# Kernel optimization log

Measured on AMD Instinct MI355X. Metric: run time of the kernel, lower is better.

The kernel has to match this reference:

```python
import jax, jax.numpy as jnp
import numpy as np

B, T, C = 4, 2048, 768
N_HEAD = 12
HS = C // N_HEAD

def setup_inputs() -> dict:
    key = jax.random.key(0)
    ks = jax.random.split(key, 5)
    s = 0.02
    return {
        "x": jax.random.normal(ks[0], (B, T, C), dtype=jnp.float32),
        "w_attn": jax.random.normal(ks[1], (C, 3 * C), dtype=jnp.float32) * s,
        "b_attn": jnp.zeros((3 * C,), dtype=jnp.float32),
        "w_proj": jax.random.normal(ks[2], (C, C), dtype=jnp.float32) * s,
        "b_proj": jnp.zeros((C,), dtype=jnp.float32),
    }

def reference(x, w_attn, b_attn, w_proj, b_proj):
    Bx, Tx, Cx = x.shape
    qkv = x @ w_attn + b_attn                      # [B,T,3C]
    q, k, v = jnp.split(qkv, 3, axis=-1)
    # [B,H,T,hs]
    q = q.reshape(Bx, Tx, N_HEAD, HS).transpose(0, 2, 1, 3)
    k = k.reshape(Bx, Tx, N_HEAD, HS).transpose(0, 2, 1, 3)
    v = v.reshape(Bx, Tx, N_HEAD, HS).transpose(0, 2, 1, 3)
    att = jnp.einsum('bhqd,bhkd->bhqk', q, k) * (1.0 / jnp.sqrt(jnp.float32(HS)))
    mask = jnp.tril(jnp.ones((Tx, Tx), dtype=bool))  # causal
    att = jnp.where(mask, att, jnp.float32(-jnp.inf))
    att = jax.nn.softmax(att, axis=-1)
    y = jnp.einsum('bhqk,bhkd->bhqd', att, v)
    y = y.transpose(0, 2, 1, 3).reshape(Bx, Tx, Cx)
    return y @ w_proj + b_proj
```

## Files before the change

### kernel.cpp

```cpp
#include <hip/hip_runtime.h>

#define BB 4
#define TT 2048
#define CC 768
#define QKVW 2304
#define NHH 12
#define HSS 64
#define NQT64 (TT / 64)

typedef __attribute__((ext_vector_type(4))) float floatx4;
typedef __attribute__((ext_vector_type(8))) short shortx8;
typedef __attribute__((ext_vector_type(4))) short shortx4;

__device__ __forceinline__ unsigned short f2bf(float f) {
  union { float f; unsigned int u; } cv; cv.f = f;
  unsigned int u = cv.u;
  u += 0x7FFFu + ((u >> 16) & 1u);
  return (unsigned short)(u >> 16);
}
__device__ __forceinline__ unsigned short bfp(float f) {
  union { float f; unsigned int u; } cv; cv.f = f;
  return (unsigned short)((cv.u + 0x8000u) >> 16);
}
__device__ __forceinline__ unsigned short bft(float f) {
  union { float f; unsigned int u; } cv; cv.f = f;
  return (unsigned short)(cv.u >> 16);
}

__device__ __forceinline__ void async_copy16(const void* g, void* l) {
  __builtin_amdgcn_global_load_lds(
      (const __attribute__((address_space(1))) unsigned int*)g,
      (__attribute__((address_space(3))) unsigned int*)l, 16, 0, 0);
}

__global__ void convert_x(const float* __restrict__ x, unsigned short* __restrict__ xb, int n4) {
  int i = blockIdx.x * blockDim.x + threadIdx.x;
  const int stride = gridDim.x * blockDim.x;
  for (; i < n4; i += stride) {
    float4 v = ((const float4*)x)[i];
    shortx4 s;
    s.x = (short)f2bf(v.x); s.y = (short)f2bf(v.y);
    s.z = (short)f2bf(v.z); s.w = (short)f2bf(v.w);
    ((shortx4*)xb)[i] = s;
  }
}

__global__ __launch_bounds__(256)
void transpose_w(const float* __restrict__ w, unsigned short* __restrict__ wt, int K, int N) {
  __shared__ short tile[64 * 68];
  const int n0 = blockIdx.x * 64, k0 = blockIdx.y * 64;
  const int tid = threadIdx.x;
  {
    const int tr = tid >> 4, tc = (tid & 15) * 4;
#pragma unroll
    for (int i = 0; i < 4; ++i) {
      float4 v = *(const float4*)(w + (size_t)(k0 + tr + 16 * i) * N + n0 + tc);
      short* d = &tile[(tr + 16 * i) * 68 + tc];
      d[0] = (short)f2bf(v.x); d[1] = (short)f2bf(v.y);
      d[2] = (short)f2bf(v.z); d[3] = (short)f2bf(v.w);
    }
  }
  __syncthreads();
  {
    const int wr = tid >> 3, wc = (tid & 7) * 8;
#pragma unroll
    for (int j = 0; j < 2; ++j) {
      const int n = wr + 32 * j;
      shortx8 s;
#pragma unroll
      for (int e = 0; e < 8; ++e) s[e] = tile[(wc + e) * 68 + n];
      *(shortx8*)(wt + (size_t)(n0 + n) * K + k0 + wc) = s;
    }
  }
}

__global__ __launch_bounds__(256)
void transpose_v(const unsigned short* __restrict__ qkv, unsigned short* __restrict__ Vt) {
  __shared__ short tile[64 * 72];
  const int t0 = blockIdx.x * 64;
  const int bh = blockIdx.y;
  const int b = bh / NHH, h = bh % NHH;
  const int tid = threadIdx.x;
  {
    const int tr = tid >> 3, tc = (tid & 7) * 8;
#pragma unroll
    for (int i = 0; i < 2; ++i) {
      shortx8 v = *(const shortx8*)(qkv + ((size_t)(b * TT + t0 + tr + 32 * i)) * QKVW + 2 * CC + h * HSS + tc);
      *(shortx8*)&tile[(tr + 32 * i) * 72 + tc] = v;
    }
  }
  __syncthreads();
  {
    const int dr = tid >> 3, tc = (tid & 7) * 8;
    const int base = (tc & 32) + ((tc >> 3) & 3) * 4;
#pragma unroll
    for (int j = 0; j < 2; ++j) {
      const int d = dr + 32 * j;
      shortx8 s;
#pragma unroll
      for (int e = 0; e < 8; ++e)
        s[e] = tile[(base + (e >> 2) * 16 + (e & 3)) * 72 + d];
      *(shortx8*)(Vt + ((size_t)bh * HSS + d) * TT + t0 + tc) = s;
    }
  }
}

template<bool OUT_BF16, bool QSCALE>
__global__ __launch_bounds__(256)
void gemm_tn(const unsigned short* __restrict__ A, const unsigned short* __restrict__ Bt,
             const float* __restrict__ bias, void* __restrict__ Cp, int M, int N, int K) {
  __shared__ short As[3][128 * 32];
  __shared__ short Bs[3][128 * 32];
  const int tid = threadIdx.x, lane = tid & 63, wave = tid >> 6;
  const int row = lane & 15, quad = lane >> 4;
  const int wm = (wave >> 1) * 64, wn = (wave & 1) * 64;
  const int m0 = blockIdx.x * 128, n0 = blockIdx.y * 128;

  floatx4 acc[4][4] = {};

  const int lr = lane >> 2;
  const int csrc = (lane & 3) ^ ((lr >> 1) & 3);
  const int sr = wave * 32 + lr;
  const unsigned short* aP = A + (size_t)(m0 + sr) * K + csrc * 8;
  const unsigned short* bP = Bt + (size_t)(n0 + sr) * K + csrc * 8;
  const int sOff = (wave * 32) * 32;

  const int qsw = (quad ^ ((row >> 1) & 3)) * 8;

  const int nk = K >> 5;

  auto stage = [&](int t, int bi) {
#pragma unroll
    for (int i = 0; i < 2; ++i) {
      async_copy16(aP + (size_t)(16 * i) * K + t * 32, &As[bi][sOff + i * 512]);
      async_copy16(bP + (size_t)(16 * i) * K + t * 32, &Bs[bi][sOff + i * 512]);
    }
  };

  stage(0, 0);
  if (nk > 1) stage(1, 1);
  int cb = 0;
  for (int t = 0; t < nk; ++t) {
    int pb = cb + 2; if (pb >= 3) pb -= 3;
    if (t + 2 < nk) {
      stage(t + 2, pb);
      asm volatile("s_waitcnt vmcnt(8)" ::: "memory");
    } else if (t + 1 < nk) {
      asm volatile("s_waitcnt vmcnt(4)" ::: "memory");
    } else {
      asm volatile("s_waitcnt vmcnt(0)" ::: "memory");
    }
    __builtin_amdgcn_sched_barrier(0);
    __builtin_amdgcn_s_barrier();
    __builtin_amdgcn_sched_barrier(0);
    {
      shortx8 af[4], bf[4];
#pragma unroll
      for (int g = 0; g < 4; ++g) {
        af[g] = *(const shortx8*)&As[cb][(wm + g * 16 + row) * 32 + qsw];
        bf[g] = *(const shortx8*)&Bs[cb][(wn + g * 16 + row) * 32 + qsw];
      }
#pragma unroll
      for (int mg = 0; mg < 4; ++mg)
#pragma unroll
        for (int ng = 0; ng < 4; ++ng)
          acc[mg][ng] = __builtin_amdgcn_mfma_f32_16x16x32_bf16(af[mg], bf[ng], acc[mg][ng], 0, 0, 0);
    }
    __builtin_amdgcn_sched_barrier(0);
    __builtin_amdgcn_s_barrier();
    __builtin_amdgcn_sched_barrier(0);
    cb = (cb + 1 == 3) ? 0 : cb + 1;
  }

#pragma unroll
  for (int mg = 0; mg < 4; ++mg) {
    const int m = m0 + wm + mg * 16 + quad * 4;
#pragma unroll
    for (int ng = 0; ng < 4; ++ng) {
      const int n = n0 + wn + ng * 16 + row;
      const float bv = bias[n];
      const float scl = (QSCALE && n < CC) ? 0.180336881f : 1.0f;
#pragma unroll
      for (int r = 0; r < 4; ++r) {
        const float val = (acc[mg][ng][r] + bv) * scl;
        if (OUT_BF16) ((unsigned short*)Cp)[(size_t)(m + r) * N + n] = f2bf(val);
        else          ((float*)Cp)[(size_t)(m + r) * N + n] = val;
      }
    }
  }
}

__global__ __launch_bounds__(256)
void attn_kernel(const unsigned short* __restrict__ qkv, const unsigned short* __restrict__ Vt,
                 unsigned short* __restrict__ y) {
  constexpr int STR = 72;
  __shared__ short Kd[2][64 * STR];
  __shared__ short Vd[2][64 * STR];

  const int id = blockIdx.x;
  const int xcd = id & 7;
  const int slot = id >> 3;
  const int qt = NQT64 - 1 - slot / 6;
  const int gl = slot % 6;
  const int g = xcd * 6 + gl;
  const int h = g % NHH, b = g / NHH;
  const int bh = b * NHH + h;
  const int tid = threadIdx.x, lane = tid & 63, wave = tid >> 6;
  const int row = lane & 15, quad = lane >> 4;
  const int qhalf = wave & 1;
  const int khalf = wave >> 1;

  const int srow = tid >> 3;
  const int scol = (tid & 7) * 8;
  const unsigned short* kSrc = qkv + ((size_t)(b * TT)) * QKVW + CC + h * HSS;
  const unsigned short* vSrc = Vt + ((size_t)bh * HSS) * TT;

  const shortx8 ones8 = {(short)0x3F80, (short)0x3F80, (short)0x3F80, (short)0x3F80,
                         (short)0x3F80, (short)0x3F80, (short)0x3F80, (short)0x3F80};

  const int qb0 = qt * 64 + qhalf * 32;
  const int nk = qt + 1;

  shortx8 qf[2][2];
#pragma unroll
  for (int qg = 0; qg < 2; ++qg) {
    const unsigned short* qp = qkv + ((size_t)(b * TT) + qb0 + qg * 16 + row) * QKVW + h * HSS;
    qf[qg][0] = *(const shortx8*)(qp + quad * 8);
    qf[qg][1] = *(const shortx8*)(qp + 32 + quad * 8);
  }

  floatx4 lf[2] = {(floatx4)(0.0f), (floatx4)(0.0f)};
  floatx4 o[2][4];
#pragma unroll
  for (int qg = 0; qg < 2; ++qg)
#pragma unroll
    for (int dg = 0; dg < 4; ++dg) o[qg][dg] = (floatx4)(0.0f);

  shortx8 kr[2], vr[2];
#pragma unroll
  for (int i = 0; i < 2; ++i) {
    kr[i] = *(const shortx8*)(kSrc + (size_t)(srow + 32 * i) * QKVW + scol);
    vr[i] = *(const shortx8*)(vSrc + (size_t)(srow + 32 * i) * TT + scol);
  }
#pragma unroll
  for (int i = 0; i < 2; ++i) {
    *(shortx8*)&Kd[0][(srow + 32 * i) * STR + scol] = kr[i];
    *(shortx8*)&Vd[0][(srow + 32 * i) * STR + scol] = vr[i];
  }
  __syncthreads();

  for (int kt = 0; kt < nk; ++kt) {
    const int cur = kt & 1;
    if (kt + 1 < nk) {
#pragma unroll
      for (int i = 0; i < 2; ++i) {
        kr[i] = *(const shortx8*)(kSrc + (size_t)((kt + 1) * 64 + srow + 32 * i) * QKVW + scol);
        vr[i] = *(const shortx8*)(vSrc + (size_t)(srow + 32 * i) * TT + (kt + 1) * 64 + scol);
      }
    }
    {
      const short* Kc = &Kd[cur][0];
      const short* Vc = &Vd[cur][0];
      shortx4 pfr[2][2];
#pragma unroll
      for (int mg = 0; mg < 2; ++mg) {
        const int krow = khalf * 32 + mg * 16 + row;
        const shortx8 kf0 = *(const shortx8*)&Kc[krow * STR + quad * 8];
        const shortx8 kf1 = *(const shortx8*)&Kc[krow * STR + 32 + quad * 8];
#pragma unroll
        for (int qg = 0; qg < 2; ++qg) {
          floatx4 t = __builtin_amdgcn_mfma_f32_16x16x32_bf16(kf0, qf[qg][0], (floatx4)(0.0f), 0, 0, 0);
          t = __builtin_amdgcn_mfma_f32_16x16x32_bf16(kf1, qf[qg][1], t, 0, 0, 0);
          if (kt == qt) {
            const int kg = kt * 64 + khalf * 32 + mg * 16 + quad * 4;
            const int qv = qb0 + qg * 16 + row;
#pragma unroll
            for (int r = 0; r < 4; ++r)
              if (kg + r > qv) t[r] = -1e30f;
          }
          shortx4 pk;
#pragma unroll
          for (int r = 0; r < 4; ++r) pk[r] = (short)bft(__builtin_amdgcn_exp2f(t[r]));
          pfr[qg][mg] = pk;
        }
      }
      shortx8 pk8[2];
#pragma unroll
      for (int qg = 0; qg < 2; ++qg) {
        pk8[qg] = __builtin_shufflevector(pfr[qg][0], pfr[qg][1], 0, 1, 2, 3, 4, 5, 6, 7);
        lf[qg] = __builtin_amdgcn_mfma_f32_16x16x32_bf16(pk8[qg], ones8, lf[qg], 0, 0, 0);
      }
#pragma unroll
      for (int dg = 0; dg < 4; ++dg) {
        const shortx8 vf = *(const shortx8*)&Vc[(dg * 16 + row) * STR + khalf * 32 + quad * 8];
#pragma unroll
        for (int qg = 0; qg < 2; ++qg)
          o[qg][dg] = __builtin_amdgcn_mfma_f32_16x16x32_bf16(pk8[qg], vf, o[qg][dg], 0, 0, 0);
      }
    }
    if (kt + 1 < nk) {
      const int nb = (kt + 1) & 1;
#pragma unroll
      for (int i = 0; i < 2; ++i) {
        *(shortx8*)&Kd[nb][(srow + 32 * i) * STR + scol] = kr[i];
        *(shortx8*)&Vd[nb][(srow + 32 * i) * STR + scol] = vr[i];
      }
    }
    __syncthreads();
  }

  floatx4* red4 = (floatx4*)(&Kd[0][0]);
  const int rbase = (qhalf * 64 + lane) * 11;
  if (khalf) {
#pragma unroll
    for (int qg = 0; qg < 2; ++qg) {
#pragma unroll
      for (int dg = 0; dg < 4; ++dg) red4[rbase + qg * 4 + dg] = o[qg][dg];
      red4[rbase + 8 + qg] = lf[qg];
    }
  }
  __syncthreads();
  if (!khalf) {
#pragma unroll
    for (int qg = 0; qg < 2; ++qg) {
#pragma unroll
      for (int dg = 0; dg < 4; ++dg) o[qg][dg] += red4[rbase + qg * 4 + dg];
      lf[qg] += red4[rbase + 8 + qg];
    }
#pragma unroll
    for (int qg = 0; qg < 2; ++qg) {
#pragma unroll
      for (int r = 0; r < 4; ++r) {
        const float lo = 1.0f / lf[qg][r];
        unsigned short* yp = y + ((size_t)(b * TT) + qb0 + qg * 16 + quad * 4 + r) * CC + h * HSS;
#pragma unroll
        for (int dg = 0; dg < 4; ++dg)
          yp[dg * 16 + row] = bfp(o[qg][dg][r] * lo);
      }
    }
  }
}

extern "C" void kernel_launch(void* const* d_in, const int* in_sizes, int n_in,
                              void* d_out, int out_size, void* d_ws, size_t ws_size,
                              hipStream_t stream) {
  const float* x      = (const float*)d_in[0];
  const float* w_attn = (const float*)d_in[1];
  const float* b_attn = (const float*)d_in[2];
  const float* w_proj = (const float*)d_in[3];
  const float* b_proj = (const float*)d_in[4];
  float* out = (float*)d_out;

  char* ws = (char*)d_ws;
  unsigned short* xb  = (unsigned short*)ws;
  unsigned short* y   = (unsigned short*)ws;
  unsigned short* qkv = (unsigned short*)(ws + 12582912);
  unsigned short* wta = (unsigned short*)(ws + 50331648);
  unsigned short* Vt  = (unsigned short*)(ws + 50331648);
  unsigned short* wtp = (unsigned short*)(ws + 62914560);

  const int M = BB * TT;

  convert_x<<<1024, 256, 0, stream>>>(x, xb, (M * CC) / 4);
  transpose_w<<<dim3(QKVW / 64, CC / 64), 256, 0, stream>>>(w_attn, wta, CC, QKVW);
  transpose_w<<<dim3(CC / 64, CC / 64), 256, 0, stream>>>(w_proj, wtp, CC, CC);

  gemm_tn<true, true><<<dim3(M / 128, QKVW / 128), 256, 0, stream>>>(
      xb, wta, b_attn, (void*)qkv, M, QKVW, CC);

  transpose_v<<<dim3(TT / 64, BB * NHH), 256, 0, stream>>>(qkv, Vt);

  attn_kernel<<<dim3(NQT64 * NHH * BB), 256, 0, stream>>>(qkv, Vt, y);

  gemm_tn<false, false><<<dim3(M / 128, CC / 128), 256, 0, stream>>>(
      y, wtp, b_proj, (void*)out, M, CC, CC);
}
```

Measured before the change: 201.1 us.

## Use async global-to-LDS copies with triple buffering and XOR swizzle in attention

```diff
diff --git a/kernel.cpp b/kernel.cpp
--- a/kernel.cpp
+++ b/kernel.cpp
@@ -193,9 +193,8 @@
 __global__ __launch_bounds__(256)
 void attn_kernel(const unsigned short* __restrict__ qkv, const unsigned short* __restrict__ Vt,
                  unsigned short* __restrict__ y) {
-  constexpr int STR = 72;
-  __shared__ short Kd[2][64 * STR];
-  __shared__ short Vd[2][64 * STR];
+  __shared__ short Ksh[3][64 * 64];
+  __shared__ short Vsh[3][64 * 64];
 
   const int id = blockIdx.x;
   const int xcd = id & 7;
@@ -210,8 +209,6 @@
   const int qhalf = wave & 1;
   const int khalf = wave >> 1;
 
-  const int srow = tid >> 3;
-  const int scol = (tid & 7) * 8;
   const unsigned short* kSrc = qkv + ((size_t)(b * TT)) * QKVW + CC + h * HSS;
   const unsigned short* vSrc = Vt + ((size_t)bh * HSS) * TT;
 
@@ -220,6 +217,29 @@
 
   const int qb0 = qt * 64 + qhalf * 32;
   const int nk = qt + 1;
+
+  const int lr8 = lane >> 3;
+  const int csw = ((lane & 7) ^ lr8) * 8;
+  size_t kOff[2], vOff[2];
+#pragma unroll
+  for (int i = 0; i < 2; ++i) {
+    const int r = wave * 16 + i * 8 + lr8;
+    kOff[i] = (size_t)r * QKVW + csw;
+    vOff[i] = (size_t)r * TT + csw;
+  }
+  const int sBase = (wave * 16) * 64;
+
+  const int r7 = row & 7;
+  int kR[2][2], vR[4];
+#pragma unroll
+  for (int mg = 0; mg < 2; ++mg) {
+    const int krow = khalf * 32 + mg * 16 + row;
+    kR[mg][0] = krow * 64 + ((quad ^ r7) * 8);
+    kR[mg][1] = krow * 64 + (((quad + 4) ^ r7) * 8);
+  }
+#pragma unroll
+  for (int dg = 0; dg < 4; ++dg)
+    vR[dg] = (dg * 16 + row) * 64 + (((khalf * 4 + quad) ^ r7) * 8);
 
   shortx8 qf[2][2];
 #pragma unroll
@@ -228,6 +248,7 @@
     qf[qg][0] = *(const shortx8*)(qp + quad * 8);
     qf[qg][1] = *(const shortx8*)(qp + 32 + quad * 8);
   }
+  asm volatile("s_waitcnt vmcnt(0)" ::: "memory");
 
   floatx4 lf[2] = {(floatx4)(0.0f), (floatx4)(0.0f)};
   floatx4 o[2][4];
@@ -236,37 +257,39 @@
 #pragma unroll
     for (int dg = 0; dg < 4; ++dg) o[qg][dg] = (floatx4)(0.0f);
 
-  shortx8 kr[2], vr[2];
-#pragma unroll
-  for (int i = 0; i < 2; ++i) {
-    kr[i] = *(const shortx8*)(kSrc + (size_t)(srow + 32 * i) * QKVW + scol);
-    vr[i] = *(const shortx8*)(vSrc + (size_t)(srow + 32 * i) * TT + scol);
-  }
-#pragma unroll
-  for (int i = 0; i < 2; ++i) {
-    *(shortx8*)&Kd[0][(srow + 32 * i) * STR + scol] = kr[i];
-    *(shortx8*)&Vd[0][(srow + 32 * i) * STR + scol] = vr[i];
-  }
-  __syncthreads();
-
+  auto stage = [&](int t, int bi) {
+#pragma unroll
+    for (int i = 0; i < 2; ++i) {
+      async_copy16(kSrc + (size_t)(t * 64) * QKVW + kOff[i], &Ksh[bi][sBase + i * 512]);
+      async_copy16(vSrc + (size_t)(t * 64) + vOff[i],        &Vsh[bi][sBase + i * 512]);
+    }
+  };
+
+  stage(0, 0);
+  if (nk > 1) stage(1, 1);
+  int cb = 0;
   for (int kt = 0; kt < nk; ++kt) {
-    const int cur = kt & 1;
-    if (kt + 1 < nk) {
-#pragma unroll
-      for (int i = 0; i < 2; ++i) {
-        kr[i] = *(const shortx8*)(kSrc + (size_t)((kt + 1) * 64 + srow + 32 * i) * QKVW + scol);
-        vr[i] = *(const shortx8*)(vSrc + (size_t)(srow + 32 * i) * TT + (kt + 1) * 64 + scol);
-      }
-    }
+    int pb = cb + 2; if (pb >= 3) pb -= 3;
+    if (kt + 2 < nk) {
+      stage(kt + 2, pb);
+      asm volatile("s_waitcnt vmcnt(8)" ::: "memory");
+    } else if (kt + 1 < nk) {
+      asm volatile("s_waitcnt vmcnt(4)" ::: "memory");
+    } else {
+      asm volatile("s_waitcnt vmcnt(0)" ::: "memory");
+    }
+    __builtin_amdgcn_sched_barrier(0);
+    __builtin_amdgcn_s_barrier();
+    __builtin_amdgcn_sched_barrier(0);
     {
-      const short* Kc = &Kd[cur][0];
-      const short* Vc = &Vd[cur][0];
+      const short* Kc = &Ksh[cb][0];
+      const short* Vc = &Vsh[cb][0];
+      __builtin_amdgcn_s_setprio(1);
       shortx4 pfr[2][2];
 #pragma unroll
       for (int mg = 0; mg < 2; ++mg) {
-        const int krow = khalf * 32 + mg * 16 + row;
-        const shortx8 kf0 = *(const shortx8*)&Kc[krow * STR + quad * 8];
-        const shortx8 kf1 = *(const shortx8*)&Kc[krow * STR + 32 + quad * 8];
+        const shortx8 kf0 = *(const shortx8*)&Kc[kR[mg][0]];
+        const shortx8 kf1 = *(const shortx8*)&Kc[kR[mg][1]];
 #pragma unroll
         for (int qg = 0; qg < 2; ++qg) {
           floatx4 t = __builtin_amdgcn_mfma_f32_16x16x32_bf16(kf0, qf[qg][0], (floatx4)(0.0f), 0, 0, 0);
@@ -292,24 +315,20 @@
       }
 #pragma unroll
       for (int dg = 0; dg < 4; ++dg) {
-        const shortx8 vf = *(const shortx8*)&Vc[(dg * 16 + row) * STR + khalf * 32 + quad * 8];
+        const shortx8 vf = *(const shortx8*)&Vc[vR[dg]];
 #pragma unroll
         for (int qg = 0; qg < 2; ++qg)
           o[qg][dg] = __builtin_amdgcn_mfma_f32_16x16x32_bf16(pk8[qg], vf, o[qg][dg], 0, 0, 0);
       }
-    }
-    if (kt + 1 < nk) {
-      const int nb = (kt + 1) & 1;
-#pragma unroll
-      for (int i = 0; i < 2; ++i) {
-        *(shortx8*)&Kd[nb][(srow + 32 * i) * STR + scol] = kr[i];
-        *(shortx8*)&Vd[nb][(srow + 32 * i) * STR + scol] = vr[i];
-      }
-    }
-    __syncthreads();
-  }
-
-  floatx4* red4 = (floatx4*)(&Kd[0][0]);
+      __builtin_amdgcn_s_setprio(0);
+    }
+    __builtin_amdgcn_sched_barrier(0);
+    __builtin_amdgcn_s_barrier();
+    __builtin_amdgcn_sched_barrier(0);
+    cb = (cb + 1 == 3) ? 0 : cb + 1;
+  }
+
+  floatx4* red4 = (floatx4*)(&Ksh[0][0]);
   const int rbase = (qhalf * 64 + lane) * 11;
   if (khalf) {
 #pragma unroll
```

New measurement: 204.1 us. About the same (+1.5%).
